# Kernel tuning notes

Measured on AMD Instinct MI355X. Metric: run time of the kernel, lower is better.

The kernel has to match this reference:

```python
import jax, jax.numpy as jnp
import numpy as np

B, IN_LEN, NN, IN_DIM = 32, 28, 2048, 1
E, ND = 256, 256          # embed_dim, node_dim
H = E + ND                # hidden_dim = 512
N_LAYERS = 3
OUT_LEN = 28


def setup_inputs() -> dict:
    key = jax.random.key(0)
    ks = jax.random.split(key, 16)
    x_node = jax.random.normal(ks[0], (B, IN_LEN, NN, IN_DIM), jnp.float32)
    # x_state channels: [0]=cumulative cases, [1]=infected I, [2]=population N
    col0 = jax.random.uniform(ks[1], (B, IN_LEN, NN, 1), jnp.float32) * 100.0
    colI = jax.random.uniform(ks[2], (B, IN_LEN, NN, 1), jnp.float32) * 100.0 + 1.0
    colN = 1e4 * (1.0 + 0.1 * jax.random.uniform(ks[3], (B, IN_LEN, NN, 1), jnp.float32))
    x_state = jnp.concatenate([col0, colI, colN], axis=-1)
    node_emb = jax.random.normal(ks[4], (NN, ND), jnp.float32) * 0.05
    W_ts = jax.random.normal(ks[5], (E, IN_DIM * IN_LEN), jnp.float32) * 0.05
    b_ts = jnp.zeros((E,), jnp.float32)
    enc_W1 = jax.random.normal(ks[6], (N_LAYERS, H, H), jnp.float32) * 0.02
    enc_b1 = jnp.zeros((N_LAYERS, H), jnp.float32)
    enc_W2 = jax.random.normal(ks[7], (N_LAYERS, H, H), jnp.float32) * 0.02
    enc_b2 = jnp.zeros((N_LAYERS, H), jnp.float32)
    Wb = jax.random.normal(ks[8], (1, H), jnp.float32) * 0.05
    bb = jnp.zeros((1,), jnp.float32)
    Wg = jax.random.normal(ks[9], (1, H), jnp.float32) * 0.05
    bg = jnp.zeros((1,), jnp.float32)
    return dict(x_node=x_node, x_state=x_state, node_emb=node_emb,
                W_ts=W_ts, b_ts=b_ts, enc_W1=enc_W1, enc_b1=enc_b1,
                enc_W2=enc_W2, enc_b2=enc_b2, Wb=Wb, bb=bb, Wg=Wg, bg=bg)


def _forward(x_node, x_state, node_emb, W_ts, b_ts,
             enc_W1, enc_b1, enc_W2, enc_b2, Wb, bb, Wg, bg):
    Bn, Lh, Nn, _ = x_node.shape
    # [B,L,N,D] -> [B,N,L*D] (channel = in_dim*in_len for 1x1 conv == linear)
    flat = jnp.transpose(x_node[..., :IN_DIM], (0, 2, 1, 3)).reshape(Bn, Nn, Lh * IN_DIM)
    ts = flat @ W_ts.T + b_ts                                  # [B,N,E]
    h = jnp.concatenate(
        [ts, jnp.broadcast_to(node_emb[None], (Bn,) + node_emb.shape)], axis=-1)  # [B,N,H]
    for l in range(enc_W1.shape[0]):                            # residual MLP encoder
        z = jnp.maximum(h @ enc_W1[l].T + enc_b1[l], 0.0)
        h = h + z @ enc_W2[l].T + enc_b2[l]
    b = jax.nn.sigmoid(h @ Wb.T + bb)                           # [B,N,1] infection rate
    g = jax.nn.sigmoid(h @ Wg.T + bg)                           # [B,N,1] recovery rate

    Npop = x_state[:, -1, :, 2:3]                               # [B,N,1]
    I_hist = x_state[..., 1:2] / g[:, None]                     # [B,L,N,1]
    Iin_hist = jnp.maximum(
        I_hist[:, 1:] - I_hist[:, :-1] + x_state[:, :-1, :, 1:2], 0.0)  # [B,L-1,N,1]
    t1 = jnp.arange(Lh - 1, 0, -1, dtype=jnp.float32)
    w1 = jnp.exp(-g[:, None] * t1[None, :, None, None])         # [B,L-1,N,1]
    I_Tm1 = jnp.sum(w1 * Iin_hist, axis=1)                      # [B,N,1]
    R_Tm1 = Npop - x_state[:, -2, :, 0:1]
    S_Tm1 = Npop - I_Tm1 - R_Tm1
    Iin0 = b * S_Tm1 * I_Tm1 / Npop
    Rin0 = g * I_hist[:, -1, :, 0:1]
    Iin_hist = jnp.concatenate([Iin_hist, Iin0[:, None]], axis=1)  # [B,L,N,1]
    S = S_Tm1 - Iin0
    t2 = jnp.arange(Lh, 0, -1, dtype=jnp.float32)
    w2 = jnp.exp(-g[:, None] * t2[None, :, None, None])
    I = jnp.sum(w2 * Iin_hist, axis=1)                          # [B,N,1]
    R = R_Tm1 + Rin0

    # The torch loop recomputes sum_i exp(-g*(L-i))*Iin_i each step; exact identity:
    # I_new = exp(-g) * (I_old + Iin_new). O(T) scan instead of O(T^2).
    decay = jnp.exp(-g)

    def step(carry, _):
        S, I, R = carry
        Iin = b * S * I / Npop
        S = S - Iin
        Rin = g * I            # uses pre-update I_T, matching torch order
        I = decay * (I + Iin)
        R = R + Rin
        return (S, I, R), Rin

    _, rins = jax.lax.scan(step, (S, I, R), None, length=OUT_LEN)  # [T,B,N,1]
    return jnp.transpose(rins, (1, 0, 2, 3))                       # [B,out_len,N,1]


def reference(x_node, x_state, node_emb, W_ts, b_ts, enc_W1, enc_b1,
              enc_W2, enc_b2, Wb, bb, Wg, bg):
    return _forward(x_node, x_state, node_emb, W_ts, b_ts,
                    enc_W1, enc_b1, enc_W2, enc_b2, Wb, bb, Wg, bg)
```

## Files before the change

kernel.cpp:

```cpp
#include <hip/hip_runtime.h>
#include <hip/hip_bf16.h>
#include <math.h>

#define BATCH 32
#define IN_LEN 28
#define NN 2048
#define E 256
#define H 512
#define N_LAYERS 3
#define OUT_LEN 28
#define M_ROWS (BATCH * NN)

typedef unsigned short u16;
typedef unsigned int   u32;
typedef __attribute__((ext_vector_type(8))) short short8;
typedef __attribute__((ext_vector_type(4))) float f32x4;

__device__ __forceinline__ u16 f2h(float x) {
    union { _Float16 h; u16 u; } v; v.h = (_Float16)x; return v.u;
}
__device__ __forceinline__ float h2f(u16 u) {
    union { _Float16 h; u16 u; } v; v.u = u; return (float)v.h;
}

__device__ __forceinline__ void gload_lds16(const void* g, void* l) {
    __builtin_amdgcn_global_load_lds(
        (const __attribute__((address_space(1))) void*)g,
        (__attribute__((address_space(3))) void*)l, 16, 0, 0);
}

__global__ __launch_bounds__(256)
void k_split2(const float* __restrict__ w1, const float* __restrict__ w2,
              u16* __restrict__ hi, u16* __restrict__ lo, int nW)
{
    int i = blockIdx.x * 256 + threadIdx.x;
    float v = (i < nW) ? w1[i] : w2[i - nW];
    u16 h = f2h(v);
    hi[i] = h;
    lo[i] = f2h(v - h2f(h));
}

__global__ __launch_bounds__(256)
void k_ts(const float* __restrict__ x_node, const float* __restrict__ node_emb,
          const float* __restrict__ W_ts, const float* __restrict__ b_ts,
          u16* __restrict__ hhi, u16* __restrict__ hlo)
{
    __shared__ float xs[IN_LEN][64];
    const int tid = threadIdx.x;
    const int b   = blockIdx.y;
    const int n0  = blockIdx.x * 64;
    const int c   = tid & 127;
    const int sec = tid >> 7;

    for (int idx = tid; idx < IN_LEN * 64; idx += 256) {
        int l = idx >> 6, i = idx & 63;
        xs[l][i] = x_node[((size_t)b * IN_LEN + l) * NN + n0 + i];
    }

    float w0[IN_LEN], w1[IN_LEN];
    float bias0 = 0.f, bias1 = 0.f;
    if (sec == 0) {
        #pragma unroll
        for (int j = 0; j < IN_LEN; j++) {
            w0[j] = W_ts[(2 * c) * IN_LEN + j];
            w1[j] = W_ts[(2 * c + 1) * IN_LEN + j];
        }
        bias0 = b_ts[2 * c];
        bias1 = b_ts[2 * c + 1];
    }
    __syncthreads();

    for (int i = 0; i < 64; i++) {
        size_t row = (size_t)b * NN + n0 + i;
        u32* oh = (u32*)(hhi + row * H);
        u32* ol = (u32*)(hlo + row * H);
        float v0, v1;
        int oc;
        if (sec == 0) {
            v0 = bias0; v1 = bias1;
            #pragma unroll
            for (int j = 0; j < IN_LEN; j++) {
                float x = xs[j][i];
                v0 += x * w0[j];
                v1 += x * w1[j];
            }
            oc = c;
        } else {
            const float2 ev = *(const float2*)&node_emb[(size_t)(n0 + i) * 256 + 2 * c];
            v0 = ev.x; v1 = ev.y;
            oc = 128 + c;
        }
        u16 h0 = f2h(v0), h1 = f2h(v1);
        oh[oc] = (u32)h0 | ((u32)h1 << 16);
        ol[oc] = (u32)f2h(v0 - h2f(h0)) | ((u32)f2h(v1 - h2f(h1)) << 16);
    }
}

__global__ __launch_bounds__(256)
void k_gemm1(const u16* __restrict__ Ahi, const u16* __restrict__ Alo,
             const u16* __restrict__ Whi, const u16* __restrict__ Wlo,
             const float* __restrict__ bias, u16* __restrict__ Z)
{
    __shared__ __align__(16) u16 smem[32768];

    const int tid = threadIdx.x;
    const int ln  = tid & 63;
    const int wv  = tid >> 6;

    const int id   = blockIdx.x;
    const int c    = (id >> 3) & 3;
    const int r    = (id & 7) | ((id >> 5) << 3);
    const int row0 = r * 128;
    const int col0 = c * 128;

    const int rbase = (wv & 1) * 64;
    const int cbase = (wv >> 1) * 64;

    const int lr = ln >> 2;
    const int lc = ln & 3;

    const u16* sgsrc; int sofs; int tb;
    if      (wv == 0) { sgsrc = Ahi; sofs = 0;     tb = row0; }
    else if (wv == 1) { sgsrc = Alo; sofs = 8192;  tb = row0; }
    else if (wv == 2) { sgsrc = Whi; sofs = 16384; tb = col0; }
    else              { sgsrc = Wlo; sofs = 24576; tb = col0; }

    auto stage = [&](int p, int kt) {
        u16* dstbuf = smem + sofs + p * 4096;
        #pragma unroll
        for (int i = 0; i < 8; i++) {
            int row = i * 16 + lr;
            int sc  = lc ^ ((row >> 1) & 3);
            gload_lds16(sgsrc + (size_t)(tb + row) * H + kt + sc * 8,
                        dstbuf + i * 512);
        }
    };

    f32x4 acc[4][4];
    #pragma unroll
    for (int m = 0; m < 4; m++)
        #pragma unroll
        for (int n = 0; n < 4; n++) acc[m][n] = (f32x4)(0.f);

    stage(0, 0);

    const int wl = ln & 15;

    for (int t = 0; t < 16; t++) {
        const int p = t & 1;
        __syncthreads();
        if (t + 1 < 16) stage(1 - p, (t + 1) * 32);

        const u16* bAh = smem + 0     + p * 4096;
        const u16* bAl = smem + 8192  + p * 4096;
        const u16* bWh = smem + 16384 + p * 4096;
        const u16* bWl = smem + 24576 + p * 4096;

        short8 ahi[4], alo[4], whi[4], wlo[4];
        #pragma unroll
        for (int m = 0; m < 4; m++) {
            int rr = rbase + m * 16 + wl;
            int cc = ((ln >> 4) ^ ((rr >> 1) & 3)) * 8;
            ahi[m] = *(const short8*)&bAh[rr * 32 + cc];
            alo[m] = *(const short8*)&bAl[rr * 32 + cc];
        }
        #pragma unroll
        for (int n = 0; n < 4; n++) {
            int wr = cbase + n * 16 + wl;
            int cc = ((ln >> 4) ^ ((wr >> 1) & 3)) * 8;
            whi[n] = *(const short8*)&bWh[wr * 32 + cc];
            wlo[n] = *(const short8*)&bWl[wr * 32 + cc];
        }
        #pragma unroll
        for (int m = 0; m < 4; m++)
            #pragma unroll
            for (int n = 0; n < 4; n++) {
                acc[m][n] = __builtin_amdgcn_mfma_f32_16x16x32_f16(ahi[m], whi[n], acc[m][n], 0, 0, 0);
                acc[m][n] = __builtin_amdgcn_mfma_f32_16x16x32_f16(ahi[m], wlo[n], acc[m][n], 0, 0, 0);
                acc[m][n] = __builtin_amdgcn_mfma_f32_16x16x32_f16(alo[m], whi[n], acc[m][n], 0, 0, 0);
            }
    }

    __syncthreads();
    u16* zb = smem + wv * 4096;
    float bv[4];
    #pragma unroll
    for (int n = 0; n < 4; n++) bv[n] = bias[col0 + cbase + n * 16 + wl];
    #pragma unroll
    for (int m = 0; m < 4; m++)
        #pragma unroll
        for (int n = 0; n < 4; n++)
            #pragma unroll
            for (int rg = 0; rg < 4; rg++) {
                int row_l = m * 16 + (ln >> 4) * 4 + rg;
                zb[row_l * 64 + n * 16 + wl] =
                    f2h(fmaxf(acc[m][n][rg] + bv[n], 0.f));
            }
    const int cr = ln >> 3;
    const int cc = (ln & 7) * 8;
    #pragma unroll
    for (int p2 = 0; p2 < 8; p2++) {
        int row_l = cr + p2 * 8;
        uint4 v = *(const uint4*)&zb[row_l * 64 + cc];
        *(uint4*)&Z[(size_t)(row0 + rbase + row_l) * H + col0 + cbase + cc] = v;
    }
}

template <int HEAD>
__global__ __launch_bounds__(256)
void k_gemm2(const u16* __restrict__ Z,
             const u16* __restrict__ Whi, const u16* __restrict__ Wlo,
             const float* __restrict__ bias,
             u16* HHi, u16* HLo,
             const float* __restrict__ Wb, const float* __restrict__ Wg,
             float* __restrict__ bSum, float* __restrict__ gSum)
{
    __shared__ __align__(16) u16 smem[24576];

    const int tid = threadIdx.x;
    const int ln  = tid & 63;
    const int wv  = tid >> 6;

    const int id   = blockIdx.x;
    const int c    = (id >> 3) & 3;
    const int r    = (id & 7) | ((id >> 5) << 3);
    const int row0 = r * 128;
    const int col0 = c * 128;

    const int rbase = (wv & 1) * 64;
    const int cbase = (wv >> 1) * 64;

    const int lr = ln >> 2;
    const int lc = ln & 3;

    const u16* sgsrc; int sofs; int tb; int iofs; int niss;
    if      (wv == 0) { sgsrc = Z;   sofs = 0;     tb = row0;      iofs = 0;    niss = 4; }
    else if (wv == 3) { sgsrc = Z;   sofs = 0;     tb = row0 + 64; iofs = 2048; niss = 4; }
    else if (wv == 1) { sgsrc = Whi; sofs = 8192;  tb = col0;      iofs = 0;    niss = 8; }
    else              { sgsrc = Wlo; sofs = 16384; tb = col0;      iofs = 0;    niss = 8; }

    auto stage = [&](int p, int kt) {
        u16* dstbuf = smem + sofs + p * 4096 + iofs;
        #pragma unroll
        for (int i = 0; i < 8; i++) {
            if (i >= niss) break;
            int row = i * 16 + lr;
            int sc  = lc ^ ((row >> 1) & 3);
            gload_lds16(sgsrc + (size_t)(tb + row) * H + kt + sc * 8,
                        dstbuf + i * 512);
        }
    };

    f32x4 acc[4][4];
    #pragma unroll
    for (int m = 0; m < 4; m++)
        #pragma unroll
        for (int n = 0; n < 4; n++) acc[m][n] = (f32x4)(0.f);

    stage(0, 0);

    const int wl = ln & 15;

    for (int t = 0; t < 16; t++) {
        const int p = t & 1;
        __syncthreads();
        if (t + 1 < 16) stage(1 - p, (t + 1) * 32);

        const u16* bZ  = smem + 0     + p * 4096;
        const u16* bWh = smem + 8192  + p * 4096;
        const u16* bWl = smem + 16384 + p * 4096;

        short8 az[4], whi[4], wlo[4];
        #pragma unroll
        for (int m = 0; m < 4; m++) {
            int rr = rbase + m * 16 + wl;
            int cc = ((ln >> 4) ^ ((rr >> 1) & 3)) * 8;
            az[m] = *(const short8*)&bZ[rr * 32 + cc];
        }
        #pragma unroll
        for (int n = 0; n < 4; n++) {
            int wr = cbase + n * 16 + wl;
            int cc = ((ln >> 4) ^ ((wr >> 1) & 3)) * 8;
            whi[n] = *(const short8*)&bWh[wr * 32 + cc];
            wlo[n] = *(const short8*)&bWl[wr * 32 + cc];
        }
        #pragma unroll
        for (int m = 0; m < 4; m++)
            #pragma unroll
            for (int n = 0; n < 4; n++) {
                acc[m][n] = __builtin_amdgcn_mfma_f32_16x16x32_f16(az[m], whi[n], acc[m][n], 0, 0, 0);
                acc[m][n] = __builtin_amdgcn_mfma_f32_16x16x32_f16(az[m], wlo[n], acc[m][n], 0, 0, 0);
            }
    }

    __syncthreads();
    float* fb = (float*)smem + wv * 2048;

    const int cr  = ln >> 3;
    const int ccl = (ln & 7) * 4;
    float pb[8], pg[8];
    if (HEAD) {
        #pragma unroll
        for (int p2 = 0; p2 < 8; p2++) { pb[p2] = 0.f; pg[p2] = 0.f; }
    }

    #pragma unroll
    for (int nh = 0; nh < 2; nh++) {
        #pragma unroll
        for (int m = 0; m < 4; m++)
            #pragma unroll
            for (int j = 0; j < 2; j++)
                #pragma unroll
                for (int rg = 0; rg < 4; rg++) {
                    int row_l = m * 16 + (ln >> 4) * 4 + rg;
                    fb[row_l * 32 + j * 16 + wl] = acc[m][nh * 2 + j][rg];
                }
        const int gc0 = col0 + cbase + nh * 32 + ccl;
        float4 bv = *(const float4*)&bias[gc0];
        float4 hb, hg;
        if (HEAD) {
            hb = *(const float4*)&Wb[gc0];
            hg = *(const float4*)&Wg[gc0];
        }
        #pragma unroll
        for (int p2 = 0; p2 < 8; p2++) {
            int row_l = cr + p2 * 8;
            size_t gidx = (size_t)(row0 + rbase + row_l) * H + gc0;
            uint2 uh = *(const uint2*)(HHi + gidx);
            uint2 ul = *(const uint2*)(HLo + gidx);
            float4 a = *(const float4*)&fb[row_l * 32 + ccl];
            float v0 = a.x + bv.x + h2f((u16)(uh.x & 0xFFFF)) + h2f((u16)(ul.x & 0xFFFF));
            float v1 = a.y + bv.y + h2f((u16)(uh.x >> 16))    + h2f((u16)(ul.x >> 16));
            float v2 = a.z + bv.z + h2f((u16)(uh.y & 0xFFFF)) + h2f((u16)(ul.y & 0xFFFF));
            float v3 = a.w + bv.w + h2f((u16)(uh.y >> 16))    + h2f((u16)(ul.y >> 16));
            if (HEAD) {
                pb[p2] += v0 * hb.x + v1 * hb.y + v2 * hb.z + v3 * hb.w;
                pg[p2] += v0 * hg.x + v1 * hg.y + v2 * hg.z + v3 * hg.w;
            } else {
                u16 h0 = f2h(v0), h1 = f2h(v1), h2 = f2h(v2), h3 = f2h(v3);
                uint2 oh, ol;
                oh.x = (u32)h0 | ((u32)h1 << 16);
                oh.y = (u32)h2 | ((u32)h3 << 16);
                ol.x = (u32)f2h(v0 - h2f(h0)) | ((u32)f2h(v1 - h2f(h1)) << 16);
                ol.y = (u32)f2h(v2 - h2f(h2)) | ((u32)f2h(v3 - h2f(h3)) << 16);
                *(uint2*)(HHi + gidx) = oh;
                *(uint2*)(HLo + gidx) = ol;
            }
        }
    }

    if (HEAD) {
        #pragma unroll
        for (int p2 = 0; p2 < 8; p2++) {
            float sb = pb[p2], sg = pg[p2];
            #pragma unroll
            for (int off = 1; off < 8; off <<= 1) {
                sb += __shfl_xor(sb, off);
                sg += __shfl_xor(sg, off);
            }
            if ((ln & 7) == 0) {
                int grow = row0 + rbase + cr + p2 * 8;
                atomicAdd(&bSum[grow], sb);
                atomicAdd(&gSum[grow], sg);
            }
        }
    }
}

__global__ __launch_bounds__(256)
void k_sir(const float* __restrict__ x_state,
           const float* __restrict__ bSum, const float* __restrict__ gSum,
           const float* __restrict__ bb, const float* __restrict__ bg,
           float* __restrict__ out)
{
    const int row = blockIdx.x * 256 + threadIdx.x;
    const int bb_ = row / NN;
    const int n   = row % NN;

    const float g = 1.f / (1.f + expf(-(gSum[row] + bg[0])));
    const float b = 1.f / (1.f + expf(-(bSum[row] + bb[0])));
    const float d = expf(-g);

    const float* xs = x_state + ((size_t)bb_ * IN_LEN) * (NN * 3) + (size_t)n * 3;

    float x1_prev = xs[1];
    float Ih_prev = x1_prev / g;
    float acc = 0.f;
    #pragma unroll 4
    for (int t = 1; t <= IN_LEN - 1; ++t) {
        float x1 = xs[(size_t)t * (NN * 3) + 1];
        float Ih = x1 / g;
        float Iin = fmaxf(Ih - Ih_prev + x1_prev, 0.f);
        acc = acc * d + Iin;
        Ih_prev = Ih;
        x1_prev = x1;
    }
    float ITm1 = acc * d;
    float Npop = xs[(size_t)(IN_LEN - 1) * (NN * 3) + 2];
    float RTm1 = Npop - xs[(size_t)(IN_LEN - 2) * (NN * 3) + 0];
    float STm1 = Npop - ITm1 - RTm1;
    float Iin0 = b * STm1 * ITm1 / Npop;
    float S = STm1 - Iin0;
    float I = d * (ITm1 + Iin0);

    float* op = out + ((size_t)bb_ * OUT_LEN) * NN + n;
    #pragma unroll 4
    for (int k = 0; k < OUT_LEN; k++) {
        float Iin = b * S * I / Npop;
        S = S - Iin;
        float Rin = g * I;
        I = d * (I + Iin);
        op[(size_t)k * NN] = Rin;
    }
}

extern "C" void kernel_launch(void* const* d_in, const int* in_sizes, int n_in,
                              void* d_out, int out_size, void* d_ws, size_t ws_size,
                              hipStream_t stream)
{
    const float* x_node   = (const float*)d_in[0];
    const float* x_state  = (const float*)d_in[1];
    const float* node_emb = (const float*)d_in[2];
    const float* W_ts     = (const float*)d_in[3];
    const float* b_ts     = (const float*)d_in[4];
    const float* enc_W1   = (const float*)d_in[5];
    const float* enc_b1   = (const float*)d_in[6];
    const float* enc_W2   = (const float*)d_in[7];
    const float* enc_b2   = (const float*)d_in[8];
    const float* Wb       = (const float*)d_in[9];
    const float* bb       = (const float*)d_in[10];
    const float* Wg       = (const float*)d_in[11];
    const float* bg       = (const float*)d_in[12];
    float* out = (float*)d_out;

    u16* hhi   = (u16*)d_ws;
    u16* hlo   = hhi + (size_t)M_ROWS * H;
    u16* wHi   = hlo + (size_t)M_ROWS * H;
    u16* wLo   = wHi + (size_t)6 * H * H;
    float* bSum = (float*)(wLo + (size_t)6 * H * H);
    float* gSum = bSum + M_ROWS;
    u16* z     = (u16*)(gSum + M_ROWS);

    size_t used  = (size_t)((char*)z - (char*)d_ws);
    size_t avail = (ws_size > used) ? ws_size - used : 0;
    long long chunkLL = (long long)(avail / (H * sizeof(u16))) & ~1023LL;
    int chunk = (chunkLL > M_ROWS) ? M_ROWS : (int)chunkLL;
    if (chunk < 1024) chunk = 1024;

    hipMemsetAsync(bSum, 0, 2 * (size_t)M_ROWS * sizeof(float), stream);

    const int nW = N_LAYERS * H * H;
    k_split2<<<2 * nW / 256, 256, 0, stream>>>(enc_W1, enc_W2, wHi, wLo, nW);

    k_ts<<<dim3(NN / 64, BATCH), 256, 0, stream>>>(x_node, node_emb, W_ts, b_ts, hhi, hlo);

    for (int l = 0; l < N_LAYERS; l++) {
        const u16* W1hi = wHi + (size_t)l * H * H;
        const u16* W1lo = wLo + (size_t)l * H * H;
        const u16* W2hi = wHi + (size_t)nW + (size_t)l * H * H;
        const u16* W2lo = wLo + (size_t)nW + (size_t)l * H * H;
        const float* b1 = enc_b1 + (size_t)l * H;
        const float* b2 = enc_b2 + (size_t)l * H;
        for (int r = 0; r < M_ROWS; r += chunk) {
            int rows = (M_ROWS - r < chunk) ? (M_ROWS - r) : chunk;
            u16* hrhi = hhi + (size_t)r * H;
            u16* hrlo = hlo + (size_t)r * H;
            int nblk = (rows / 128) * 4;
            k_gemm1<<<nblk, 256, 0, stream>>>(hrhi, hrlo, W1hi, W1lo, b1, z);
            if (l < N_LAYERS - 1)
                k_gemm2<0><<<nblk, 256, 0, stream>>>(z, W2hi, W2lo, b2, hrhi, hrlo,
                                                     Wb, Wg, bSum + r, gSum + r);
            else
                k_gemm2<1><<<nblk, 256, 0, stream>>>(z, W2hi, W2lo, b2, hrhi, hrlo,
                                                     Wb, Wg, bSum + r, gSum + r);
        }
    }

    k_sir<<<M_ROWS / 256, 256, 0, stream>>>(x_state, bSum, gSum, bb, bg, out);
}
```

Baseline: 770.0 us.

## Deepen activation prefetch pipeline with explicit vmcnt waits in GEMM kernels

Activation (A/Z) tiles now use a 3-stage (gemm1) or 4-stage (gemm2) LDS ring buffer, while weight tiles stay double-buffered. __syncthreads is replaced by per-wave s_waitcnt vmcnt counts plus a raw s_barrier. Activation loads can then run two or three k-steps ahead and hide global latency on the streaming operand. This costs more LDS per block, which may lower occupancy, and the hand-written vmcnt counts are fragile.

Measured after the change: 766.1 us. No clear change (-0.5%).

```diff
diff --git a/kernel.cpp b/kernel.cpp
--- a/kernel.cpp
+++ b/kernel.cpp
@@ -16,6 +16,9 @@
 typedef __attribute__((ext_vector_type(8))) short short8;
 typedef __attribute__((ext_vector_type(4))) float f32x4;
 
+#define WAITV(N)  asm volatile("s_waitcnt vmcnt(" #N ")" ::: "memory")
+#define BARRIER() __builtin_amdgcn_s_barrier()
+
 __device__ __forceinline__ u16 f2h(float x) {
     union { _Float16 h; u16 u; } v; v.h = (_Float16)x; return v.u;
 }
@@ -101,7 +104,7 @@
              const u16* __restrict__ Whi, const u16* __restrict__ Wlo,
              const float* __restrict__ bias, u16* __restrict__ Z)
 {
-    __shared__ __align__(16) u16 smem[32768];
+    __shared__ __align__(16) u16 smem[40960];
 
     const int tid = threadIdx.x;
     const int ln  = tid & 63;
@@ -121,9 +124,9 @@
 
     const u16* sgsrc; int sofs; int tb;
     if      (wv == 0) { sgsrc = Ahi; sofs = 0;     tb = row0; }
-    else if (wv == 1) { sgsrc = Alo; sofs = 8192;  tb = row0; }
-    else if (wv == 2) { sgsrc = Whi; sofs = 16384; tb = col0; }
-    else              { sgsrc = Wlo; sofs = 24576; tb = col0; }
+    else if (wv == 1) { sgsrc = Alo; sofs = 12288; tb = row0; }
+    else if (wv == 2) { sgsrc = Whi; sofs = 24576; tb = col0; }
+    else              { sgsrc = Wlo; sofs = 32768; tb = col0; }
 
     auto stage = [&](int p, int kt) {
         u16* dstbuf = smem + sofs + p * 4096;
@@ -143,18 +146,22 @@
         for (int n = 0; n < 4; n++) acc[m][n] = (f32x4)(0.f);
 
     stage(0, 0);
+    if (wv < 2) stage(1, 32);
 
     const int wl = ln & 15;
 
     for (int t = 0; t < 16; t++) {
-        const int p = t & 1;
-        __syncthreads();
-        if (t + 1 < 16) stage(1 - p, (t + 1) * 32);
-
-        const u16* bAh = smem + 0     + p * 4096;
-        const u16* bAl = smem + 8192  + p * 4096;
-        const u16* bWh = smem + 16384 + p * 4096;
-        const u16* bWl = smem + 24576 + p * 4096;
+        if (wv < 2) { if (t < 15) { WAITV(8); } else { WAITV(0); } }
+        else        { WAITV(0); }
+        BARRIER();
+        if (wv < 2) { if (t + 2 < 16) stage((t + 2) % 3, (t + 2) * 32); }
+        else        { if (t + 1 < 16) stage((t + 1) & 1, (t + 1) * 32); }
+
+        const int pa = t % 3, pw = t & 1;
+        const u16* bAh = smem + 0     + pa * 4096;
+        const u16* bAl = smem + 12288 + pa * 4096;
+        const u16* bWh = smem + 24576 + pw * 4096;
+        const u16* bWl = smem + 32768 + pw * 4096;
 
         short8 ahi[4], alo[4], whi[4], wlo[4];
         #pragma unroll
@@ -215,7 +222,7 @@
              const float* __restrict__ Wb, const float* __restrict__ Wg,
              float* __restrict__ bSum, float* __restrict__ gSum)
 {
-    __shared__ __align__(16) u16 smem[24576];
+    __shared__ __align__(16) u16 smem[32768];
 
     const int tid = threadIdx.x;
     const int ln  = tid & 63;
@@ -234,10 +241,11 @@
     const int lc = ln & 3;
 
     const u16* sgsrc; int sofs; int tb; int iofs; int niss;
+    const bool zw = (wv == 0) || (wv == 3);
     if      (wv == 0) { sgsrc = Z;   sofs = 0;     tb = row0;      iofs = 0;    niss = 4; }
     else if (wv == 3) { sgsrc = Z;   sofs = 0;     tb = row0 + 64; iofs = 2048; niss = 4; }
-    else if (wv == 1) { sgsrc = Whi; sofs = 8192;  tb = col0;      iofs = 0;    niss = 8; }
-    else              { sgsrc = Wlo; sofs = 16384; tb = col0;      iofs = 0;    niss = 8; }
+    else if (wv == 1) { sgsrc = Whi; sofs = 16384; tb = col0;      iofs = 0;    niss = 8; }
+    else              { sgsrc = Wlo; sofs = 24576; tb = col0;      iofs = 0;    niss = 8; }
 
     auto stage = [&](int p, int kt) {
         u16* dstbuf = smem + sofs + p * 4096 + iofs;
@@ -258,17 +266,24 @@
         for (int n = 0; n < 4; n++) acc[m][n] = (f32x4)(0.f);
 
     stage(0, 0);
+    if (zw) { stage(1, 32); stage(2, 64); }
 
     const int wl = ln & 15;
 
     for (int t = 0; t < 16; t++) {
-        const int p = t & 1;
-        __syncthreads();
-        if (t + 1 < 16) stage(1 - p, (t + 1) * 32);
-
-        const u16* bZ  = smem + 0     + p * 4096;
-        const u16* bWh = smem + 8192  + p * 4096;
-        const u16* bWl = smem + 16384 + p * 4096;
+        if (zw) {
+            if      (t < 14) { WAITV(8); }
+            else if (t == 14){ WAITV(4); }
+            else             { WAITV(0); }
+        } else { WAITV(0); }
+        BARRIER();
+        if (zw) { if (t + 3 < 16) stage((t + 3) & 3, (t + 3) * 32); }
+        else    { if (t + 1 < 16) stage((t + 1) & 1, (t + 1) * 32); }
+
+        const int pz = t & 3, pw = t & 1;
+        const u16* bZ  = smem + 0     + pz * 4096;
+        const u16* bWh = smem + 16384 + pw * 4096;
+        const u16* bWl = smem + 24576 + pw * 4096;
 
         short8 az[4], whi[4], wlo[4];
         #pragma unroll
```
